# Performance work log

Hardware: AMD Instinct MI355X
Metric: run time of the kernel (lower is better)

Reference implementation:

```python
import jax, jax.numpy as jnp
import numpy as np

NUM_HEADS = 16
HEAD_DIM = 128
D_MODEL = 2048
BATCH = 2
SEQ = 2048


def setup_inputs() -> dict:
    key = jax.random.key(0)
    ks = jax.random.split(key, 6)
    x = jax.random.normal(ks[0], (BATCH, SEQ, D_MODEL), dtype=jnp.float32)
    # RoPE tables (real/imag parts of freqs_cis), shape [S, HEAD_DIM//2]
    pos = jnp.arange(SEQ, dtype=jnp.float32)[:, None]
    inv_freq = 1.0 / (10000.0 ** (jnp.arange(0, HEAD_DIM, 2, dtype=jnp.float32) / HEAD_DIM))
    ang = pos * inv_freq[None, :]
    freq_cos = jnp.cos(ang)
    freq_sin = jnp.sin(ang)
    scale = 1.0 / np.sqrt(D_MODEL)
    wq = jax.random.normal(ks[1], (D_MODEL, NUM_HEADS * HEAD_DIM), dtype=jnp.float32) * scale
    wk = jax.random.normal(ks[2], (D_MODEL, NUM_HEADS * HEAD_DIM), dtype=jnp.float32) * scale
    wv = jax.random.normal(ks[3], (D_MODEL, NUM_HEADS * HEAD_DIM), dtype=jnp.float32) * scale
    wo = jax.random.normal(ks[4], (NUM_HEADS * HEAD_DIM, D_MODEL), dtype=jnp.float32) * scale
    return {"x": x, "freq_cos": freq_cos, "freq_sin": freq_sin,
            "wq": wq, "wk": wk, "wv": wv, "wo": wo}


def _rotate_half(t):
    half = t.shape[-1] // 2
    return jnp.concatenate([-t[..., half:], t[..., :half]], axis=-1)


def _apply_rope(q, k, freq_cos, freq_sin):
    # q, k: [B, H, S, D]; freq_cos/sin: [S_total, D//2]
    q = q.astype(jnp.float32)
    k = k.astype(jnp.float32)
    S = q.shape[2]
    cos = jnp.concatenate([freq_cos[:S], freq_cos[:S]], axis=-1)[None, None]  # [1,1,S,D]
    sin = jnp.concatenate([freq_sin[:S], freq_sin[:S]], axis=-1)[None, None]
    q_out = q * cos + _rotate_half(q) * sin
    k_out = k * cos + _rotate_half(k) * sin
    return q_out, k_out


def reference(x, freq_cos, freq_sin, wq, wk, wv, wo):
    B, S, D = x.shape
    H, hd = NUM_HEADS, HEAD_DIM
    q = (x @ wq).reshape(B, S, H, hd).transpose(0, 2, 1, 3)  # [B,H,S,hd]
    k = (x @ wk).reshape(B, S, H, hd).transpose(0, 2, 1, 3)
    v = (x @ wv).reshape(B, S, H, hd).transpose(0, 2, 1, 3)
    q, k = _apply_rope(q, k, freq_cos, freq_sin)
    # explicit causal attention (faithful to CPU/GPU path)
    logits = jnp.einsum('bhqd,bhkd->bhqk', q, k) / jnp.sqrt(jnp.float32(hd))
    mask = jnp.tril(jnp.ones((S, S), dtype=jnp.float32))
    logits = jnp.where(mask[None, None, :, :], logits, -1e10)
    weights = jax.nn.softmax(logits, axis=-1)
    out = jnp.einsum('bhqk,bhkd->bhqd', weights, v)  # [B,H,S,hd]
    out = out.transpose(0, 2, 1, 3).reshape(B, S, H * hd)
    return out @ wo
```

## Files before the change

kernel.cpp:

```cpp
#include <hip/hip_runtime.h>

typedef unsigned short u16;
typedef unsigned int u32;
typedef __attribute__((ext_vector_type(8))) short bf16x8;
typedef __attribute__((ext_vector_type(4))) short bf16x4;
typedef __attribute__((ext_vector_type(4))) float f32x4;

#define MFMA(a, b, c) __builtin_amdgcn_mfma_f32_16x16x32_bf16(a, b, c, 0, 0, 0)
#define ASYNC16(g, l)                                                        \
  __builtin_amdgcn_global_load_lds(                                          \
      (const __attribute__((address_space(1))) u32*)(g),                     \
      (__attribute__((address_space(3))) u32*)(l), 16, 0, 0)

__device__ __forceinline__ float b2f(u16 u) {
  union { u32 i; float f; } x; x.i = ((u32)u) << 16; return x.f;
}
__device__ __forceinline__ u16 f2b(float f) {
  union { float f; u32 i; } x; x.f = f;
  return (u16)((x.i + 0x7fff + ((x.i >> 16) & 1)) >> 16);
}
__device__ __forceinline__ f32x4 fzero4() { f32x4 z = {0.f, 0.f, 0.f, 0.f}; return z; }

__global__ __launch_bounds__(256) void cvt_x(const float* __restrict__ src,
                                             u16* __restrict__ dst) {
  const int i = (blockIdx.x * 256 + threadIdx.x) * 4;
  const f32x4 v = *(const f32x4*)(src + i);
  bf16x4 o;
  o[0] = (short)f2b(v[0]); o[1] = (short)f2b(v[1]);
  o[2] = (short)f2b(v[2]); o[3] = (short)f2b(v[3]);
  *(bf16x4*)(dst + i) = o;
}

__global__ __launch_bounds__(256) void wtrans_f32(const float* __restrict__ src,
                                                  u16* __restrict__ dst) {
  __shared__ u16 tile[64][65];
  const int k0 = blockIdx.y * 64, n0 = blockIdx.x * 64;
  const int t = threadIdx.x;
  const int tr = t >> 3, tc = t & 7;

#pragma unroll
  for (int hh = 0; hh < 2; ++hh) {
    const int k = tr + hh * 32;
    const float* p = src + (size_t)(k0 + k) * 2048 + n0 + tc * 8;
    const f32x4 a = *(const f32x4*)(p);
    const f32x4 b = *(const f32x4*)(p + 4);
#pragma unroll
    for (int j = 0; j < 4; ++j) tile[k][tc * 8 + j] = f2b(a[j]);
#pragma unroll
    for (int j = 0; j < 4; ++j) tile[k][tc * 8 + 4 + j] = f2b(b[j]);
  }
  __syncthreads();
#pragma unroll
  for (int hh = 0; hh < 2; ++hh) {
    const int n = tr + hh * 32;
    bf16x8 v;
#pragma unroll
    for (int j = 0; j < 8; ++j) v[j] = (short)tile[tc * 8 + j][n];
    *(bf16x8*)(dst + (size_t)(n0 + n) * 2048 + k0 + tc * 8) = v;
  }
}

__global__ __launch_bounds__(256) void wtrans3(const float* __restrict__ wq,
                                               const float* __restrict__ wk,
                                               const float* __restrict__ wv,
                                               u16* __restrict__ wTall) {
  __shared__ u16 tile[64][65];
  const int z = blockIdx.z;
  const float* src = (z == 0) ? wq : (z == 1) ? wk : wv;
  u16* dst = wTall + (size_t)z * 2048 * 2048;
  const int k0 = blockIdx.y * 64, n0 = blockIdx.x * 64;
  const int t = threadIdx.x;
  const int tr = t >> 3, tc = t & 7;

#pragma unroll
  for (int hh = 0; hh < 2; ++hh) {
    const int k = tr + hh * 32;
    const float* p = src + (size_t)(k0 + k) * 2048 + n0 + tc * 8;
    const f32x4 a = *(const f32x4*)(p);
    const f32x4 b = *(const f32x4*)(p + 4);
#pragma unroll
    for (int j = 0; j < 4; ++j) tile[k][tc * 8 + j] = f2b(a[j]);
#pragma unroll
    for (int j = 0; j < 4; ++j) tile[k][tc * 8 + 4 + j] = f2b(b[j]);
  }
  __syncthreads();
#pragma unroll
  for (int hh = 0; hh < 2; ++hh) {
    const int n = tr + hh * 32;
    bf16x8 v;
#pragma unroll
    for (int j = 0; j < 8; ++j) v[j] = (short)tile[tc * 8 + j][n];
    *(bf16x8*)(dst + (size_t)(n0 + n) * 2048 + k0 + tc * 8) = v;
  }
}

__device__ __forceinline__ void gemm_mainloop(const u16* __restrict__ A,
                                              const u16* __restrict__ Bt,
                                              int K, int m0, int n0,
                                              u16* lA, u16* lB,
                                              f32x4 acc[4][4]) {
  const int tid = threadIdx.x;
  const int lane = tid & 63;
  const int wave = tid >> 6;
  const int quad = lane >> 4;
  const int l16 = lane & 15;
  const int wr = wave >> 1, wc = wave & 1;

  const int srow = lane >> 2;
  const int scol = (lane & 3) * 8;
  const u16* ga0 = A + (size_t)(m0 + (wave * 2 + 0) * 16 + srow) * K + scol;
  const u16* ga1 = A + (size_t)(m0 + (wave * 2 + 1) * 16 + srow) * K + scol;
  const u16* gb0 = Bt + (size_t)(n0 + (wave * 2 + 0) * 16 + srow) * K + scol;
  const u16* gb1 = Bt + (size_t)(n0 + (wave * 2 + 1) * 16 + srow) * K + scol;
  u16* la0 = lA + (wave * 2 + 0) * 512;
  u16* la1 = lA + (wave * 2 + 1) * 512;
  u16* lb0 = lB + (wave * 2 + 0) * 512;
  u16* lb1 = lB + (wave * 2 + 1) * 512;

  for (int k0 = 0; k0 < K; k0 += 32) {
    ASYNC16(ga0 + k0, la0);
    ASYNC16(ga1 + k0, la1);
    ASYNC16(gb0 + k0, lb0);
    ASYNC16(gb1 + k0, lb1);
    __syncthreads();
    bf16x8 af[4], bfr[4];
#pragma unroll
    for (int mb = 0; mb < 4; ++mb)
      af[mb] = *(const bf16x8*)(lA + ((wr * 64 + mb * 16 + l16) * 32 + quad * 8));
#pragma unroll
    for (int nb = 0; nb < 4; ++nb)
      bfr[nb] = *(const bf16x8*)(lB + ((wc * 64 + nb * 16 + l16) * 32 + quad * 8));
#pragma unroll
    for (int mb = 0; mb < 4; ++mb)
#pragma unroll
      for (int nb = 0; nb < 4; ++nb)
        acc[mb][nb] = MFMA(af[mb], bfr[nb], acc[mb][nb]);
    __syncthreads();
  }
}

__global__ __launch_bounds__(256) void gemm_qkv(const u16* __restrict__ x,
                                                const u16* __restrict__ wT,
                                                u16* __restrict__ qkv) {
  __shared__ u16 lA[128 * 32];
  __shared__ u16 lB[128 * 32];
  f32x4 acc[4][4];
#pragma unroll
  for (int i = 0; i < 4; ++i)
#pragma unroll
    for (int j = 0; j < 4; ++j) acc[i][j] = fzero4();

  const int m0 = blockIdx.y * 128, n0 = blockIdx.x * 128;
  gemm_mainloop(x, wT, 2048, m0, n0, lA, lB, acc);

  const int lane = threadIdx.x & 63, wave = threadIdx.x >> 6;
  const int quad = lane >> 4, l16 = lane & 15;
  const int wr = wave >> 1, wc = wave & 1;
#pragma unroll
  for (int mb = 0; mb < 4; ++mb)
#pragma unroll
    for (int nb = 0; nb < 4; ++nb)
#pragma unroll
      for (int r = 0; r < 4; ++r) {
        const int row = m0 + wr * 64 + mb * 16 + quad * 4 + r;
        const int col = n0 + wc * 64 + nb * 16 + l16;
        const int b = row >> 11, s = row & 2047;
        const int which = col >> 11, rem = col & 2047;
        const int hh = rem >> 7, d = rem & 127;
        const size_t idx = (size_t)which * ((size_t)4096 * 2048) +
                           (((size_t)(b * 16 + hh) * 2048 + s) * 128 + d);
        qkv[idx] = f2b(acc[mb][nb][r]);
      }
}

__global__ __launch_bounds__(256) void gemm_out(const u16* __restrict__ Oin,
                                                const u16* __restrict__ woT,
                                                float* __restrict__ out) {
  __shared__ u16 lA[128 * 32];
  __shared__ u16 lB[128 * 32];
  f32x4 acc[4][4];
#pragma unroll
  for (int i = 0; i < 4; ++i)
#pragma unroll
    for (int j = 0; j < 4; ++j) acc[i][j] = fzero4();

  const int m0 = blockIdx.y * 128, n0 = blockIdx.x * 128;
  gemm_mainloop(Oin, woT, 2048, m0, n0, lA, lB, acc);

  const int lane = threadIdx.x & 63, wave = threadIdx.x >> 6;
  const int quad = lane >> 4, l16 = lane & 15;
  const int wr = wave >> 1, wc = wave & 1;
#pragma unroll
  for (int mb = 0; mb < 4; ++mb)
#pragma unroll
    for (int nb = 0; nb < 4; ++nb)
#pragma unroll
      for (int r = 0; r < 4; ++r) {
        const int row = m0 + wr * 64 + mb * 16 + quad * 4 + r;
        const int col = n0 + wc * 64 + nb * 16 + l16;
        out[(size_t)row * 2048 + col] = acc[mb][nb][r];
      }
}

__global__ __launch_bounds__(256) void rope_kernel(u16* __restrict__ Q,
                                                   u16* __restrict__ K,
                                                   const float* __restrict__ fcos,
                                                   const float* __restrict__ fsin) {
  const int i = blockIdx.x * 256 + threadIdx.x;
  const int d = i & 63;
  const int s = (i >> 6) & 2047;
  const int bh = i >> 17;
  const size_t base = ((size_t)bh * 2048 + s) * 128;
  const float c = fcos[s * 64 + d];
  const float sn = fsin[s * 64 + d];
  const float qs = 0.08838834764831845f;

  const float q0 = b2f(Q[base + d]), q1 = b2f(Q[base + d + 64]);
  Q[base + d] = f2b((q0 * c - q1 * sn) * qs);
  Q[base + d + 64] = f2b((q1 * c + q0 * sn) * qs);
  const float k0 = b2f(K[base + d]), k1 = b2f(K[base + d + 64]);
  K[base + d] = f2b(k0 * c - k1 * sn);
  K[base + d + 64] = f2b(k1 * c + k0 * sn);
}

__global__ __launch_bounds__(256) void attn2(const u16* __restrict__ Q,
                                             const u16* __restrict__ K,
                                             const u16* __restrict__ V,
                                             u16* __restrict__ O) {
  __shared__ u16 lK[64 * 136];
  __shared__ u16 lV[128 * 72];
  __shared__ u16 lP[4 * 16 * 72];

  const int bh = blockIdx.y;
  const int b = bh >> 4, h = bh & 15;
  const u16* Qh = Q + (size_t)bh * 2048 * 128;
  const u16* Kh = K + (size_t)bh * 2048 * 128;
  const u16* Vh = V + (size_t)bh * 2048 * 128;

  const int tid = threadIdx.x;
  const int lane = tid & 63, wave = tid >> 6;
  const int quad = lane >> 4, l16 = lane & 15;
  const int np = tid & 31, dg = tid >> 5;
  const int d0 = dg * 16, r0 = np * 2;
  const int krow = tid >> 4, kj = tid & 15;
  u16* lPw = lP + wave * (16 * 72);

  bf16x8 kreg[4], vreg[4];

#pragma unroll
  for (int half = 0; half < 2; ++half) {
    const int qt = (half == 0) ? (int)blockIdx.x : 31 - (int)blockIdx.x;
    const int q0 = qt * 64;

    bf16x8 qf[4];
    {
      const u16* qrow = Qh + (size_t)(q0 + wave * 16 + l16) * 128 + quad * 8;
#pragma unroll
      for (int kc = 0; kc < 4; ++kc) qf[kc] = *(const bf16x8*)(qrow + kc * 32);
    }

    float m_i[4], l_i[4];
    f32x4 accO[8];
#pragma unroll
    for (int r = 0; r < 4; ++r) { m_i[r] = -1e30f; l_i[r] = 0.f; }
#pragma unroll
    for (int db = 0; db < 8; ++db) accO[db] = fzero4();

    {
#pragma unroll
      for (int i = 0; i < 4; ++i)
        kreg[i] = *(const bf16x8*)(Kh + (size_t)(krow + 16 * i) * 128 + kj * 8);
      const u16* vp = Vh + (size_t)r0 * 128 + d0;
      vreg[0] = *(const bf16x8*)(vp);
      vreg[1] = *(const bf16x8*)(vp + 8);
      vreg[2] = *(const bf16x8*)(vp + 128);
      vreg[3] = *(const bf16x8*)(vp + 136);
    }

    for (int n0 = 0; n0 <= q0; n0 += 64) {
#pragma unroll
      for (int i = 0; i < 4; ++i)
        *(bf16x8*)(lK + (krow + 16 * i) * 136 + kj * 8) = kreg[i];
#pragma unroll
      for (int j = 0; j < 8; ++j) {
        const u32 lo = (u16)vreg[0][j], hi = (u16)vreg[2][j];
        *(u32*)(lV + (d0 + j) * 72 + r0) = lo | (hi << 16);
      }
#pragma unroll
      for (int j = 0; j < 8; ++j) {
        const u32 lo = (u16)vreg[1][j], hi = (u16)vreg[3][j];
        *(u32*)(lV + (d0 + 8 + j) * 72 + r0) = lo | (hi << 16);
      }
      __syncthreads();

      if (n0 + 64 <= q0) {
        const int nn = n0 + 64;
#pragma unroll
        for (int i = 0; i < 4; ++i)
          kreg[i] = *(const bf16x8*)(Kh + (size_t)(nn + krow + 16 * i) * 128 + kj * 8);
        const u16* vp = Vh + (size_t)(nn + r0) * 128 + d0;
        vreg[0] = *(const bf16x8*)(vp);
        vreg[1] = *(const bf16x8*)(vp + 8);
        vreg[2] = *(const bf16x8*)(vp + 128);
        vreg[3] = *(const bf16x8*)(vp + 136);
      }

      f32x4 sf[4];
#pragma unroll
      for (int nb = 0; nb < 4; ++nb) {
        sf[nb] = fzero4();
#pragma unroll
        for (int kc = 0; kc < 4; ++kc) {
          bf16x8 kf = *(const bf16x8*)(lK + ((nb * 16 + l16) * 136 + kc * 32 + quad * 8));
          sf[nb] = MFMA(qf[kc], kf, sf[nb]);
        }
      }
      if (n0 == q0) {
#pragma unroll
        for (int nb = 0; nb < 4; ++nb)
#pragma unroll
          for (int r = 0; r < 4; ++r) {
            const int rowl = wave * 16 + quad * 4 + r;
            const int coll = nb * 16 + l16;
            if (coll > rowl) sf[nb][r] = -1e30f;
          }
      }
      float pr[4][4], alpha[4];
#pragma unroll
      for (int r = 0; r < 4; ++r) {
        float mx = fmaxf(fmaxf(sf[0][r], sf[1][r]), fmaxf(sf[2][r], sf[3][r]));
#pragma unroll
        for (int off = 1; off < 16; off <<= 1) mx = fmaxf(mx, __shfl_xor(mx, off));
        const float mn = fmaxf(m_i[r], mx);
        alpha[r] = __expf(m_i[r] - mn);
        m_i[r] = mn;
        float rs = 0.f;
#pragma unroll
        for (int nb = 0; nb < 4; ++nb) {
          const float p = __expf(sf[nb][r] - mn);
          pr[nb][r] = p;
          rs += p;
        }
#pragma unroll
        for (int off = 1; off < 16; off <<= 1) rs += __shfl_xor(rs, off);
        l_i[r] = l_i[r] * alpha[r] + rs;
      }
#pragma unroll
      for (int db = 0; db < 8; ++db)
#pragma unroll
        for (int r = 0; r < 4; ++r) accO[db][r] *= alpha[r];

#pragma unroll
      for (int nb = 0; nb < 4; ++nb)
#pragma unroll
        for (int r = 0; r < 4; ++r)
          lPw[(quad * 4 + r) * 72 + nb * 16 + l16] = f2b(pr[nb][r]);
      __syncthreads();

#pragma unroll
      for (int kc2 = 0; kc2 < 2; ++kc2) {
        bf16x8 pf = *(const bf16x8*)(lPw + (l16 * 72 + kc2 * 32 + quad * 8));
#pragma unroll
        for (int db = 0; db < 8; ++db) {
          bf16x8 vf = *(const bf16x8*)(lV + ((db * 16 + l16) * 72 + kc2 * 32 + quad * 8));
          accO[db] = MFMA(pf, vf, accO[db]);
        }
      }
      __syncthreads();
    }

#pragma unroll
    for (int r = 0; r < 4; ++r) {
      const float inv = 1.0f / l_i[r];
      const int srow = q0 + wave * 16 + quad * 4 + r;
      u16* orow = O + ((size_t)b * 2048 + srow) * 2048 + h * 128;
#pragma unroll
      for (int db = 0; db < 8; ++db)
        orow[db * 16 + l16] = f2b(accO[db][r] * inv);
    }
  }
}

extern "C" void kernel_launch(void* const* d_in, const int* in_sizes, int n_in,
                              void* d_out, int out_size, void* d_ws, size_t ws_size,
                              hipStream_t stream) {
  const float* x  = (const float*)d_in[0];
  const float* fc = (const float*)d_in[1];
  const float* fs = (const float*)d_in[2];
  const float* wq = (const float*)d_in[3];
  const float* wk = (const float*)d_in[4];
  const float* wv = (const float*)d_in[5];
  const float* wo = (const float*)d_in[6];
  float* out = (float*)d_out;

  u16* ws = (u16*)d_ws;
  const size_t BUF = (size_t)4096 * 2048;
  u16* xb  = ws;
  u16* Ob  = ws;
  u16* Qb  = ws + 1 * BUF;
  u16* Kb  = ws + 2 * BUF;
  u16* Vb  = ws + 3 * BUF;
  u16* wTall = (u16*)d_out;
  u16* woT = Kb;

  hipLaunchKernelGGL(cvt_x, dim3(8192), dim3(256), 0, stream, x, xb);
  hipLaunchKernelGGL(wtrans3, dim3(32, 32, 3), dim3(256), 0, stream, wq, wk, wv, wTall);
  hipLaunchKernelGGL(gemm_qkv, dim3(48, 32), dim3(256), 0, stream, xb, wTall, Qb);
  hipLaunchKernelGGL(rope_kernel, dim3(16384), dim3(256), 0, stream, Qb, Kb, fc, fs);
  hipLaunchKernelGGL(attn2, dim3(16, 32), dim3(256), 0, stream, Qb, Kb, Vb, Ob);
  hipLaunchKernelGGL(wtrans_f32, dim3(32, 32), dim3(256), 0, stream, wo, woT);
  hipLaunchKernelGGL(gemm_out, dim3(16, 32), dim3(256), 0, stream, Ob, woT, out);
}
```

Baseline: 419.4 us.

## Enlarge attention query tile to 128 rows with 8 waves sharing K/V tiles

Result: no change. 427.0 us (+1.8%).

```diff
diff --git a/kernel.cpp b/kernel.cpp
--- a/kernel.cpp
+++ b/kernel.cpp
@@ -223,13 +223,13 @@
   K[base + d + 64] = f2b(k1 * c + k0 * sn);
 }
 
-__global__ __launch_bounds__(256) void attn2(const u16* __restrict__ Q,
+__global__ __launch_bounds__(512) void attn3(const u16* __restrict__ Q,
                                              const u16* __restrict__ K,
                                              const u16* __restrict__ V,
                                              u16* __restrict__ O) {
   __shared__ u16 lK[64 * 136];
   __shared__ u16 lV[128 * 72];
-  __shared__ u16 lP[4 * 16 * 72];
+  __shared__ u16 lP[8 * 16 * 72];
 
   const int bh = blockIdx.y;
   const int b = bh >> 4, h = bh & 15;
@@ -240,17 +240,17 @@
   const int tid = threadIdx.x;
   const int lane = tid & 63, wave = tid >> 6;
   const int quad = lane >> 4, l16 = lane & 15;
+  const int krow = tid >> 4, kj = tid & 15;
   const int np = tid & 31, dg = tid >> 5;
-  const int d0 = dg * 16, r0 = np * 2;
-  const int krow = tid >> 4, kj = tid & 15;
+  const int d0 = dg * 8, r0 = np * 2;
   u16* lPw = lP + wave * (16 * 72);
 
-  bf16x8 kreg[4], vreg[4];
+  bf16x8 kreg[2], vreg[2];
 
 #pragma unroll
   for (int half = 0; half < 2; ++half) {
-    const int qt = (half == 0) ? (int)blockIdx.x : 31 - (int)blockIdx.x;
-    const int q0 = qt * 64;
+    const int T = (half == 0) ? (int)blockIdx.x : 15 - (int)blockIdx.x;
+    const int q0 = T * 128;
 
     bf16x8 qf[4];
     {
@@ -266,43 +266,31 @@
 #pragma unroll
     for (int db = 0; db < 8; ++db) accO[db] = fzero4();
 
-    {
-#pragma unroll
-      for (int i = 0; i < 4; ++i)
-        kreg[i] = *(const bf16x8*)(Kh + (size_t)(krow + 16 * i) * 128 + kj * 8);
-      const u16* vp = Vh + (size_t)r0 * 128 + d0;
-      vreg[0] = *(const bf16x8*)(vp);
-      vreg[1] = *(const bf16x8*)(vp + 8);
-      vreg[2] = *(const bf16x8*)(vp + 128);
-      vreg[3] = *(const bf16x8*)(vp + 136);
-    }
-
-    for (int n0 = 0; n0 <= q0; n0 += 64) {
-#pragma unroll
-      for (int i = 0; i < 4; ++i)
-        *(bf16x8*)(lK + (krow + 16 * i) * 136 + kj * 8) = kreg[i];
+#pragma unroll
+    for (int i = 0; i < 2; ++i)
+      kreg[i] = *(const bf16x8*)(Kh + (size_t)(krow + 32 * i) * 128 + kj * 8);
+    vreg[0] = *(const bf16x8*)(Vh + (size_t)r0 * 128 + d0);
+    vreg[1] = *(const bf16x8*)(Vh + (size_t)(r0 + 1) * 128 + d0);
+
+    const int nend = q0 + 64;
+    for (int n0 = 0; n0 <= nend; n0 += 64) {
+#pragma unroll
+      for (int i = 0; i < 2; ++i)
+        *(bf16x8*)(lK + (krow + 32 * i) * 136 + kj * 8) = kreg[i];
 #pragma unroll
       for (int j = 0; j < 8; ++j) {
-        const u32 lo = (u16)vreg[0][j], hi = (u16)vreg[2][j];
+        const u32 lo = (u16)vreg[0][j], hi = (u16)vreg[1][j];
         *(u32*)(lV + (d0 + j) * 72 + r0) = lo | (hi << 16);
       }
-#pragma unroll
-      for (int j = 0; j < 8; ++j) {
-        const u32 lo = (u16)vreg[1][j], hi = (u16)vreg[3][j];
-        *(u32*)(lV + (d0 + 8 + j) * 72 + r0) = lo | (hi << 16);
-      }
       __syncthreads();
 
-      if (n0 + 64 <= q0) {
+      if (n0 <= q0) {
         const int nn = n0 + 64;
 #pragma unroll
-        for (int i = 0; i < 4; ++i)
-          kreg[i] = *(const bf16x8*)(Kh + (size_t)(nn + krow + 16 * i) * 128 + kj * 8);
-        const u16* vp = Vh + (size_t)(nn + r0) * 128 + d0;
-        vreg[0] = *(const bf16x8*)(vp);
-        vreg[1] = *(const bf16x8*)(vp + 8);
-        vreg[2] = *(const bf16x8*)(vp + 128);
-        vreg[3] = *(const bf16x8*)(vp + 136);
+        for (int i = 0; i < 2; ++i)
+          kreg[i] = *(const bf16x8*)(Kh + (size_t)(nn + krow + 32 * i) * 128 + kj * 8);
+        vreg[0] = *(const bf16x8*)(Vh + (size_t)(nn + r0) * 128 + d0);
+        vreg[1] = *(const bf16x8*)(Vh + (size_t)(nn + r0 + 1) * 128 + d0);
       }
 
       f32x4 sf[4];
@@ -315,13 +303,14 @@
           sf[nb] = MFMA(qf[kc], kf, sf[nb]);
         }
       }
-      if (n0 == q0) {
+      if (n0 >= q0) {
+        const int co = n0 - q0;
 #pragma unroll
         for (int nb = 0; nb < 4; ++nb)
 #pragma unroll
           for (int r = 0; r < 4; ++r) {
             const int rowl = wave * 16 + quad * 4 + r;
-            const int coll = nb * 16 + l16;
+            const int coll = co + nb * 16 + l16;
             if (coll > rowl) sf[nb][r] = -1e30f;
           }
       }
@@ -407,7 +396,7 @@
   hipLaunchKernelGGL(wtrans3, dim3(32, 32, 3), dim3(256), 0, stream, wq, wk, wv, wTall);
   hipLaunchKernelGGL(gemm_qkv, dim3(48, 32), dim3(256), 0, stream, xb, wTall, Qb);
   hipLaunchKernelGGL(rope_kernel, dim3(16384), dim3(256), 0, stream, Qb, Kb, fc, fs);
-  hipLaunchKernelGGL(attn2, dim3(16, 32), dim3(256), 0, stream, Qb, Kb, Vb, Ob);
+  hipLaunchKernelGGL(attn3, dim3(8, 32), dim3(512), 0, stream, Qb, Kb, Vb, Ob);
   hipLaunchKernelGGL(wtrans_f32, dim3(32, 32), dim3(256), 0, stream, wo, woT);
   hipLaunchKernelGGL(gemm_out, dim3(16, 32), dim3(256), 0, stream, Ob, woT, out);
 }
```
